# Kernel optimization log

Measured on AMD Instinct MI355X. Metric: run time of the kernel, lower is better.

Reference implementation:

```python
import jax, jax.numpy as jnp
import numpy as np

N_NODES = 50000
BN_EPS = 1e-5


def gcn_conv(x, W, b, src, dst):
    # PyG GCNConv: linear, add self-loops, symmetric degree normalization, scatter-add, bias.
    h = x @ W                                        # [N, D]
    n = x.shape[0]
    deg = jax.ops.segment_sum(jnp.ones(src.shape[0], x.dtype), dst,
                              num_segments=n) + 1.0  # +1 for self-loop
    dinv = jnp.where(deg > 0, jax.lax.rsqrt(deg), 0.0)
    norm = dinv[src] * dinv[dst]                     # [E]
    agg = jax.ops.segment_sum(h[src] * norm[:, None], dst, num_segments=n)
    agg = agg + h * (dinv * dinv)[:, None]           # self-loop contribution
    return agg + b


def batch_norm(x, gamma, beta):
    # training-mode BN over the node axis (biased variance, as torch)
    mu = jnp.mean(x, axis=0)
    var = jnp.mean((x - mu) ** 2, axis=0)
    return (x - mu) * jax.lax.rsqrt(var + BN_EPS) * gamma + beta


def setup_inputs() -> dict:
    key = jax.random.key(0)
    ks = jax.random.split(key, 8)
    D, C = 128, 10
    x = jax.random.normal(ks[0], (N_NODES, D), dtype=jnp.float32)
    edge_index = jax.random.randint(ks[1], (2, 640000), 0, N_NODES, dtype=jnp.int32)
    s = 1.0 / np.sqrt(D)
    return {
        "x": x,
        "edge_index": edge_index,
        "W1": jax.random.normal(ks[2], (D, D), dtype=jnp.float32) * s,
        "b1": jnp.zeros((D,), jnp.float32),
        "gamma1": jnp.ones((D,), jnp.float32),
        "beta1": jnp.zeros((D,), jnp.float32),
        "W2": jax.random.normal(ks[3], (D, D), dtype=jnp.float32) * s,
        "b2": jnp.zeros((D,), jnp.float32),
        "gamma2": jnp.ones((D,), jnp.float32),
        "beta2": jnp.zeros((D,), jnp.float32),
        "lin1_w": jax.random.normal(ks[4], (D, D), dtype=jnp.float32) * s,
        "lin1_b": jnp.zeros((D,), jnp.float32),
        "lin2_w": jax.random.normal(ks[5], (D, C), dtype=jnp.float32) * s,
        "lin2_b": jnp.zeros((C,), jnp.float32),
    }


def reference(x, edge_index, W1, b1, gamma1, beta1, W2, b2, gamma2, beta2,
              lin1_w, lin1_b, lin2_w, lin2_b):
    src, dst = edge_index[0], edge_index[1]
    # layer 1: GCNConv -> ReLU -> BN (dropout = identity at eval)
    h = jax.nn.relu(gcn_conv(x, W1, b1, src, dst))
    h = batch_norm(h, gamma1, beta1)
    # layer 2
    h = jax.nn.relu(gcn_conv(h, W2, b2, src, dst))
    h = batch_norm(h, gamma2, beta2)
    # MLP head
    h = jax.nn.relu(h @ lin1_w + lin1_b)
    logits = h @ lin2_w + lin2_b
    return jax.nn.log_softmax(logits, axis=-1)
```

## Files before the change

### kernel.cpp

```cpp
#include <hip/hip_runtime.h>
#include <hip/hip_bf16.h>
#include <math.h>

typedef unsigned int uint;
typedef unsigned short ushort;
using f32x4 = __attribute__((ext_vector_type(4))) float;
using s16x8 = __attribute__((ext_vector_type(8))) short;

#define NSLOT 64

__device__ __forceinline__ float bflo(uint u) { return __uint_as_float(u << 16); }
__device__ __forceinline__ float bfhi(uint u) { return __uint_as_float(u & 0xffff0000u); }
__device__ __forceinline__ ushort f2bf(float f) {
    uint u = __float_as_uint(f);
    return (ushort)((u + 0x7fffu + ((u >> 16) & 1u)) >> 16);
}
__device__ __forceinline__ float sel4f(float a, float b, float c, float d, int i) {
    float r = a; r = (i == 1) ? b : r; r = (i == 2) ? c : r; r = (i == 3) ? d : r; return r;
}
__device__ __forceinline__ int sel4i(int a, int b, int c, int d, int i) {
    int r = a; r = (i == 1) ? b : r; r = (i == 2) ? c : r; r = (i == 3) ? d : r; return r;
}


__global__ void deg_count(const int* __restrict__ dst, int* __restrict__ deg, int E) {
    int e = blockIdx.x * 256 + threadIdx.x;
    if (e < E) atomicAdd(&deg[dst[e]], 1);
}

__global__ __launch_bounds__(256) void deg_block_sum(const int* __restrict__ deg,
                                                     int* __restrict__ bsum, int N) {
    __shared__ int s[256];
    int i = blockIdx.x * 256 + threadIdx.x;
    s[threadIdx.x] = (i < N) ? deg[i] : 0;
    __syncthreads();
    #pragma unroll
    for (int off = 128; off > 0; off >>= 1) {
        if (threadIdx.x < off) s[threadIdx.x] += s[threadIdx.x + off];
        __syncthreads();
    }
    if (threadIdx.x == 0) bsum[blockIdx.x] = s[0];
}

__global__ __launch_bounds__(256) void scan_bsum(int* __restrict__ bsum, int nblk) {
    __shared__ int s[256];
    int t = threadIdx.x;
    s[t] = (t < nblk) ? bsum[t] : 0;
    __syncthreads();
    for (int off = 1; off < 256; off <<= 1) {
        int v = (t >= off) ? s[t - off] : 0;
        __syncthreads();
        s[t] += v;
        __syncthreads();
    }
    if (t < nblk) bsum[t] = (t == 0) ? 0 : s[t - 1];
}

__global__ __launch_bounds__(256) void fill_rowstart(const int* __restrict__ deg,
                                                     const int* __restrict__ bsum,
                                                     int* __restrict__ row_start,
                                                     int* __restrict__ cursor,
                                                     float* __restrict__ dinv, int N, int E) {
    __shared__ int s[256];
    int t = threadIdx.x;
    int i = blockIdx.x * 256 + t;
    int dg = (i < N) ? deg[i] : 0;
    s[t] = dg;
    __syncthreads();
    for (int off = 1; off < 256; off <<= 1) {
        int v = (t >= off) ? s[t - off] : 0;
        __syncthreads();
        s[t] += v;
        __syncthreads();
    }
    if (i < N) {
        int excl = bsum[blockIdx.x] + s[t] - dg;
        row_start[i] = excl;
        cursor[i] = excl;
        dinv[i] = rsqrtf((float)dg + 1.0f);
    }
    if (i == 0) row_start[N] = E;
}

__global__ void csr_fill(const int* __restrict__ src, const int* __restrict__ dst,
                         const float* __restrict__ dinv, int* __restrict__ cursor,
                         int2* __restrict__ csr2, int E) {
    int e = blockIdx.x * 256 + threadIdx.x;
    if (e >= E) return;
    int s = src[e], d = dst[e];
    int pos = atomicAdd(&cursor[d], 1);
    csr2[pos] = make_int2(s, __float_as_int(dinv[s] * dinv[d]));
}


__global__ __launch_bounds__(256) void prep_weights(const float* __restrict__ W1,
                                                    const float* __restrict__ W2,
                                                    const float* __restrict__ W3,
                                                    const float* __restrict__ l2w,
                                                    ushort* __restrict__ wt1,
                                                    ushort* __restrict__ wt2,
                                                    ushort* __restrict__ wt3,
                                                    float* __restrict__ w2t) {
    int i = blockIdx.x * 256 + threadIdx.x;
    int li = i & 16383;
    int k = li >> 7, n = li & 127;
    const float* Ws = (i < 16384) ? W1 : (i < 32768) ? W2 : W3;
    ushort* Wd = (i < 16384) ? wt1 : (i < 32768) ? wt2 : wt3;
    Wd[n * 128 + k] = f2bf(Ws[li]);
    if (i < 1280) {
        int kk = i / 10, c = i % 10;
        w2t[c * 128 + kk] = l2w[i];
    }
}


template<bool XF32, bool AFF, bool BIAS, bool RELU>
__global__ __launch_bounds__(256) void gemm_mfma(const void* __restrict__ Xv,
                                                 const float* __restrict__ scale,
                                                 const float* __restrict__ shift,
                                                 const ushort* __restrict__ Bt,
                                                 const float* __restrict__ bias,
                                                 ushort* __restrict__ Y, int N) {
    __shared__ char smem[16384 + 32768];
    char* Al = smem;
    char* Bl = smem + 16384;

    int tid = threadIdx.x;
    int brow = blockIdx.x * 64;

    {
        int n = tid >> 1, h = tid & 1;
        const uint4* srcp = (const uint4*)(Bt + n * 128 + h * 64);
        #pragma unroll
        for (int i = 0; i < 8; ++i) {
            uint4 v = srcp[i];
            int u = (h * 8 + i) ^ (n & 7);
            *(uint4*)(Bl + n * 256 + u * 16) = v;
        }
    }
    {
        int r = tid >> 2, c0 = (tid & 3) * 32;
        int row = brow + r;
        bool ok = row < N;
        uint pk[16];
        if (XF32) {
            const float* Xr = (const float*)Xv + (size_t)row * 128 + c0;
            #pragma unroll
            for (int i = 0; i < 16; ++i) {
                float f0 = ok ? Xr[i * 2] : 0.f;
                float f1 = ok ? Xr[i * 2 + 1] : 0.f;
                pk[i] = (uint)f2bf(f0) | ((uint)f2bf(f1) << 16);
            }
        } else {
            const uint* Xr = (const uint*)((const ushort*)Xv + (size_t)row * 128 + c0);
            #pragma unroll
            for (int i = 0; i < 16; ++i) {
                uint u = ok ? Xr[i] : 0u;
                float f0 = bflo(u), f1 = bfhi(u);
                if (AFF) {
                    int c = c0 + i * 2;
                    f0 = f0 * scale[c] + shift[c];
                    f1 = f1 * scale[c + 1] + shift[c + 1];
                }
                pk[i] = (uint)f2bf(f0) | ((uint)f2bf(f1) << 16);
            }
        }
        #pragma unroll
        for (int i = 0; i < 4; ++i) {
            int u = ((tid & 3) * 4 + i) ^ (r & 7);
            *(uint4*)(Al + r * 256 + u * 16) = *(uint4*)&pk[i * 4];
        }
    }
    __syncthreads();

    int lane = tid & 63, w = tid >> 6;
    int m = lane & 15, g = lane >> 4;
    int wr = w * 16;

    f32x4 acc[8];
    #pragma unroll
    for (int nt = 0; nt < 8; ++nt) acc[nt] = (f32x4){0.f, 0.f, 0.f, 0.f};

    #pragma unroll
    for (int kk = 0; kk < 4; ++kk) {
        int u = (kk * 4 + g) ^ (m & 7);
        s16x8 a = *(const s16x8*)(Al + (wr + m) * 256 + u * 16);
        #pragma unroll
        for (int nt = 0; nt < 8; ++nt) {
            s16x8 b = *(const s16x8*)(Bl + (nt * 16 + m) * 256 + u * 16);
            acc[nt] = __builtin_amdgcn_mfma_f32_16x16x32_bf16(a, b, acc[nt], 0, 0, 0);
        }
    }

    float bv[8];
    if (BIAS) {
        #pragma unroll
        for (int nt = 0; nt < 8; ++nt) bv[nt] = bias[nt * 16 + m];
    }
    #pragma unroll
    for (int i = 0; i < 4; ++i) {
        int row = brow + wr + g * 4 + i;
        if (row < N) {
            #pragma unroll
            for (int nt = 0; nt < 8; ++nt) {
                float v = acc[nt][i];
                if (BIAS) v += bv[nt];
                if (RELU) v = fmaxf(v, 0.f);
                Y[(size_t)row * 128 + nt * 16 + m] = f2bf(v);
            }
        }
    }
}


__global__ __launch_bounds__(256) void gather_fused(const ushort* __restrict__ H,
                                                    const int* __restrict__ row_start,
                                                    const int2* __restrict__ csr2,
                                                    const float* __restrict__ dinv,
                                                    const float* __restrict__ bias,
                                                    ushort* __restrict__ Y,
                                                    float* __restrict__ bnpart, int N) {
    int g = threadIdx.x >> 6, lane = threadIdx.x & 63;
    int d = lane * 2;
    float b0 = bias[d], b1 = bias[d + 1];
    float s0 = 0.f, s1 = 0.f, ss0 = 0.f, ss1 = 0.f;

    int nchunks = (N + 3) / 4;
    int chunk = blockIdx.x * 4 + g;

    if (chunk < nchunks) {
        int c = chunk * 4;
        int nn = min(4, N - c);

        int rsv = row_start[c + min(lane, nn)];
        int rs0 = __shfl(rsv, 0);
        int rs1 = __shfl(rsv, min(1, nn));
        int rs2 = __shfl(rsv, min(2, nn));
        int rs3 = __shfl(rsv, min(3, nn));
        int rs4 = __shfl(rsv, nn);

        float dvv = dinv[c + min(lane, nn - 1)];
        float dv0 = __shfl(dvv, 0);
        float dv1 = __shfl(dvv, min(1, nn - 1));
        float dv2 = __shfl(dvv, min(2, nn - 1));
        float dv3 = __shfl(dvv, min(3, nn - 1));

        uint h0 = *(const uint*)&H[(size_t)c * 128 + d];
        uint h1 = (nn > 1) ? *(const uint*)&H[(size_t)(c + 1) * 128 + d] : 0u;
        uint h2 = (nn > 2) ? *(const uint*)&H[(size_t)(c + 2) * 128 + d] : 0u;
        uint h3 = (nn > 3) ? *(const uint*)&H[(size_t)(c + 3) * 128 + d] : 0u;

        float i0_0 = bflo(h0) * dv0 * dv0 + b0, i1_0 = bfhi(h0) * dv0 * dv0 + b1;
        float i0_1 = bflo(h1) * dv1 * dv1 + b0, i1_1 = bfhi(h1) * dv1 * dv1 + b1;
        float i0_2 = bflo(h2) * dv2 * dv2 + b0, i1_2 = bfhi(h2) * dv2 * dv2 + b1;
        float i0_3 = bflo(h3) * dv3 * dv3 + b0, i1_3 = bfhi(h3) * dv3 * dv3 + b1;

        int e0 = rs0, eend = rs4;
        int seg = 0;
        int nextb = rs1;
        float a0 = i0_0, a1 = i1_0;

        for (int base = e0; base < eend; base += 64) {
            int cnt = min(64, eend - base);
            int2 me = (lane < cnt) ? csr2[base + lane] : make_int2(0, 0);
            int sl = me.x;
            float nl = __int_as_float(me.y);

            for (int j = 0; j < cnt; j += 8) {
                int mm = min(8, cnt - j);
                uint v[8]; float nr[8];
                #pragma unroll
                for (int k = 0; k < 8; ++k) {
                    int idx = min(j + k, cnt - 1);
                    int sk = __shfl(sl, idx);
                    float nk = __shfl(nl, idx);
                    nr[k] = (k < mm) ? nk : 0.f;
                    v[k] = *(const uint*)&H[(size_t)sk * 128 + d];
                }
                #pragma unroll
                for (int k = 0; k < 8; ++k) {
                    if (k < mm) {
                        int e = base + j + k;
                        while (e >= nextb) {
                            float r0 = fmaxf(a0, 0.f), r1 = fmaxf(a1, 0.f);
                            *(uint*)&Y[(size_t)(c + seg) * 128 + d] =
                                (uint)f2bf(r0) | ((uint)f2bf(r1) << 16);
                            s0 += r0; ss0 += r0 * r0; s1 += r1; ss1 += r1 * r1;
                            seg++;
                            a0 = sel4f(i0_0, i0_1, i0_2, i0_3, seg);
                            a1 = sel4f(i1_0, i1_1, i1_2, i1_3, seg);
                            nextb = sel4i(rs1, rs2, rs3, rs4, seg);
                        }
                        a0 += bflo(v[k]) * nr[k];
                        a1 += bfhi(v[k]) * nr[k];
                    }
                }
            }
        }
        for (;;) {
            float r0 = fmaxf(a0, 0.f), r1 = fmaxf(a1, 0.f);
            *(uint*)&Y[(size_t)(c + seg) * 128 + d] = (uint)f2bf(r0) | ((uint)f2bf(r1) << 16);
            s0 += r0; ss0 += r0 * r0; s1 += r1; ss1 += r1 * r1;
            seg++;
            if (seg >= nn) break;
            a0 = sel4f(i0_0, i0_1, i0_2, i0_3, seg);
            a1 = sel4f(i1_0, i1_1, i1_2, i1_3, seg);
            nextb = sel4i(rs1, rs2, rs3, rs4, seg);
        }
    }

    float* bp = bnpart + (size_t)(blockIdx.x & (NSLOT - 1)) * 256;
    __shared__ float red[4][128];
    red[g][d] = s0; red[g][d + 1] = s1;
    __syncthreads();
    if (g == 0) {
        atomicAdd(&bp[d],     red[0][d] + red[1][d] + red[2][d] + red[3][d]);
        atomicAdd(&bp[d + 1], red[0][d + 1] + red[1][d + 1] + red[2][d + 1] + red[3][d + 1]);
    }
    __syncthreads();
    red[g][d] = ss0; red[g][d + 1] = ss1;
    __syncthreads();
    if (g == 0) {
        atomicAdd(&bp[128 + d],     red[0][d] + red[1][d] + red[2][d] + red[3][d]);
        atomicAdd(&bp[128 + d + 1], red[0][d + 1] + red[1][d + 1] + red[2][d + 1] + red[3][d + 1]);
    }
}

__global__ void bnfinalize(float* __restrict__ bnpart,
                           const float* __restrict__ gamma, const float* __restrict__ beta,
                           float* __restrict__ scale, float* __restrict__ shift, float invN) {
    int d = threadIdx.x;
    float sum = 0.f, ss = 0.f;
    #pragma unroll 8
    for (int s = 0; s < NSLOT; ++s) {
        sum += bnpart[s * 256 + d];
        ss  += bnpart[s * 256 + 128 + d];
        bnpart[s * 256 + d] = 0.f;
        bnpart[s * 256 + 128 + d] = 0.f;
    }
    float mu  = sum * invN;
    float var = ss * invN - mu * mu;
    float sc  = gamma[d] * rsqrtf(var + 1e-5f);
    scale[d] = sc;
    shift[d] = beta[d] - mu * sc;
}


__global__ __launch_bounds__(256) void head_ls(const ushort* __restrict__ H,
                                               const float* __restrict__ W2t,
                                               const float* __restrict__ b2,
                                               float* __restrict__ OUT, int N) {
    int wv = threadIdx.x >> 6, lane = threadIdx.x & 63;
    int row = blockIdx.x * 4 + wv;
    if (row >= N) return;
    uint hv = *(const uint*)&H[(size_t)row * 128 + lane * 2];
    float h0 = bflo(hv), h1 = bfhi(hv);
    float logit[10];
    #pragma unroll
    for (int c = 0; c < 10; ++c) {
        float2 w = *(const float2*)&W2t[c * 128 + lane * 2];
        float p = h0 * w.x + h1 * w.y;
        #pragma unroll
        for (int off = 32; off > 0; off >>= 1) p += __shfl_xor(p, off, 64);
        logit[c] = p + b2[c];
    }
    float m = logit[0];
    #pragma unroll
    for (int c = 1; c < 10; ++c) m = fmaxf(m, logit[c]);
    float sum = 0.f;
    #pragma unroll
    for (int c = 0; c < 10; ++c) sum += expf(logit[c] - m);
    float lse = m + logf(sum);
    if (lane < 10) OUT[(size_t)row * 10 + lane] = logit[lane] - lse;
}


static inline char* align16(char* p) { return (char*)(((uintptr_t)p + 15) & ~(uintptr_t)15); }

extern "C" void kernel_launch(void* const* d_in, const int* in_sizes, int n_in,
                              void* d_out, int out_size, void* d_ws, size_t ws_size,
                              hipStream_t stream) {
    const float* x    = (const float*)d_in[0];
    const int*   ei   = (const int*)d_in[1];
    const float* W1   = (const float*)d_in[2];
    const float* b1   = (const float*)d_in[3];
    const float* g1   = (const float*)d_in[4];
    const float* be1  = (const float*)d_in[5];
    const float* W2   = (const float*)d_in[6];
    const float* b2   = (const float*)d_in[7];
    const float* g2   = (const float*)d_in[8];
    const float* be2  = (const float*)d_in[9];
    const float* l1w  = (const float*)d_in[10];
    const float* l1b  = (const float*)d_in[11];
    const float* l2w  = (const float*)d_in[12];
    const float* l2b  = (const float*)d_in[13];
    float* out = (float*)d_out;

    int N = in_sizes[0] / 128;
    int E = in_sizes[1] / 2;
    const int* srcp = ei;
    const int* dstp = ei + E;

    char* w = (char*)d_ws;
    ushort* bufA  = (ushort*)w;  w = align16(w + (size_t)N * 128 * 2);
    ushort* bufB  = (ushort*)w;  w = align16(w + (size_t)N * 128 * 2);
    int*   degc   = (int*)w;     w += (size_t)N * 4;
    float* bnpart = (float*)w;   w = align16(w + (size_t)NSLOT * 256 * 4);
    float* dinv   = (float*)w;   w = align16(w + (size_t)N * 4);
    int*   row_st = (int*)w;     w = align16(w + (size_t)(N + 1) * 4);
    int*   cursor = (int*)w;     w = align16(w + (size_t)N * 4);
    int*   bsum   = (int*)w;     w = align16(w + 256 * 4);
    int2*  csr2   = (int2*)w;    w = align16(w + (size_t)E * 8);
    float* scale  = (float*)w;   w = align16(w + 128 * 4);
    float* shift  = (float*)w;   w = align16(w + 128 * 4);
    float* w2t    = (float*)w;   w = align16(w + 1280 * 4);
    ushort* wt1   = (ushort*)w;  w = align16(w + 16384 * 2);
    ushort* wt2   = (ushort*)w;  w = align16(w + 16384 * 2);
    ushort* wt3   = (ushort*)w;  w = align16(w + 16384 * 2);

    int eg = (E + 255) / 256;
    int ng = (N + 255) / 256;
    int gemm_grid = (N + 63) / 64;
    int nchunks = (N + 3) / 4;
    int gather_grid = (nchunks + 3) / 4;

    hipMemsetAsync(degc, 0, ((size_t)N + NSLOT * 256) * 4, stream);
    deg_count<<<eg, 256, 0, stream>>>(dstp, degc, E);
    deg_block_sum<<<ng, 256, 0, stream>>>(degc, bsum, N);
    scan_bsum<<<1, 256, 0, stream>>>(bsum, ng);
    fill_rowstart<<<ng, 256, 0, stream>>>(degc, bsum, row_st, cursor, dinv, N, E);
    csr_fill<<<eg, 256, 0, stream>>>(srcp, dstp, dinv, cursor, csr2, E);
    prep_weights<<<192, 256, 0, stream>>>(W1, W2, l1w, l2w, wt1, wt2, wt3, w2t);

    gemm_mfma<true, false, false, false><<<gemm_grid, 256, 0, stream>>>(x, nullptr, nullptr, wt1, nullptr, bufA, N);
    gather_fused<<<gather_grid, 256, 0, stream>>>(bufA, row_st, csr2, dinv, b1, bufB, bnpart, N);
    bnfinalize<<<1, 128, 0, stream>>>(bnpart, g1, be1, scale, shift, 1.0f / N);

    gemm_mfma<false, true, false, false><<<gemm_grid, 256, 0, stream>>>(bufB, scale, shift, wt2, nullptr, bufA, N);
    gather_fused<<<gather_grid, 256, 0, stream>>>(bufA, row_st, csr2, dinv, b2, bufB, bnpart, N);
    bnfinalize<<<1, 128, 0, stream>>>(bnpart, g2, be2, scale, shift, 1.0f / N);

    gemm_mfma<false, true, true, true><<<gemm_grid, 256, 0, stream>>>(bufB, scale, shift, wt3, l1b, bufA, N);
    head_ls<<<(N + 3) / 4, 256, 0, stream>>>(bufA, w2t, l2b, out, N);
}
```

Measured before the change: 360.2 us.

## Fuse MLP head into last GEMM, merge block scan, widen gather batch

Three separate changes. The final log-softmax head now runs inside the last GEMM epilogue: the ReLU output is staged in shared memory as fp32 and each wave computes logits for its 16 rows, which removes one launch and a bf16 round trip through global memory. The single-block scan of block sums is folded into fill_rowstart, where every block rescans all block sums redundantly, removing one tiny launch. The gather loop now batches 16 neighbour loads instead of 8 to keep more memory requests in flight, at the cost of higher register pressure.

```diff
diff --git a/kernel.cpp b/kernel.cpp
--- a/kernel.cpp
+++ b/kernel.cpp
@@ -42,39 +42,31 @@
     if (threadIdx.x == 0) bsum[blockIdx.x] = s[0];
 }
 
-__global__ __launch_bounds__(256) void scan_bsum(int* __restrict__ bsum, int nblk) {
-    __shared__ int s[256];
-    int t = threadIdx.x;
-    s[t] = (t < nblk) ? bsum[t] : 0;
-    __syncthreads();
-    for (int off = 1; off < 256; off <<= 1) {
-        int v = (t >= off) ? s[t - off] : 0;
-        __syncthreads();
-        s[t] += v;
-        __syncthreads();
-    }
-    if (t < nblk) bsum[t] = (t == 0) ? 0 : s[t - 1];
-}
-
 __global__ __launch_bounds__(256) void fill_rowstart(const int* __restrict__ deg,
                                                      const int* __restrict__ bsum,
                                                      int* __restrict__ row_start,
                                                      int* __restrict__ cursor,
-                                                     float* __restrict__ dinv, int N, int E) {
+                                                     float* __restrict__ dinv,
+                                                     int N, int E, int nblk) {
     __shared__ int s[256];
+    __shared__ int sb[256];
     int t = threadIdx.x;
     int i = blockIdx.x * 256 + t;
     int dg = (i < N) ? deg[i] : 0;
     s[t] = dg;
+    sb[t] = (t < nblk) ? bsum[t] : 0;
     __syncthreads();
     for (int off = 1; off < 256; off <<= 1) {
-        int v = (t >= off) ? s[t - off] : 0;
+        int v1 = (t >= off) ? s[t - off] : 0;
+        int v2 = (t >= off) ? sb[t - off] : 0;
         __syncthreads();
-        s[t] += v;
+        s[t] += v1;
+        sb[t] += v2;
         __syncthreads();
     }
     if (i < N) {
-        int excl = bsum[blockIdx.x] + s[t] - dg;
+        int boff = (blockIdx.x == 0) ? 0 : sb[blockIdx.x - 1];
+        int excl = boff + s[t] - dg;
         row_start[i] = excl;
         cursor[i] = excl;
         dinv[i] = rsqrtf((float)dg + 1.0f);
@@ -114,13 +106,16 @@
 }
 
 
-template<bool XF32, bool AFF, bool BIAS, bool RELU>
+template<bool XF32, bool AFF, bool BIAS, bool RELU, bool HEAD>
 __global__ __launch_bounds__(256) void gemm_mfma(const void* __restrict__ Xv,
                                                  const float* __restrict__ scale,
                                                  const float* __restrict__ shift,
                                                  const ushort* __restrict__ Bt,
                                                  const float* __restrict__ bias,
-                                                 ushort* __restrict__ Y, int N) {
+                                                 ushort* __restrict__ Y,
+                                                 const float* __restrict__ W2t,
+                                                 const float* __restrict__ b2,
+                                                 float* __restrict__ OUT, int N) {
     __shared__ char smem[16384 + 32768];
     char* Al = smem;
     char* Bl = smem + 16384;
@@ -197,17 +192,56 @@
         #pragma unroll
         for (int nt = 0; nt < 8; ++nt) bv[nt] = bias[nt * 16 + m];
     }
-    #pragma unroll
-    for (int i = 0; i < 4; ++i) {
-        int row = brow + wr + g * 4 + i;
-        if (row < N) {
+
+    if (!HEAD) {
+        #pragma unroll
+        for (int i = 0; i < 4; ++i) {
+            int row = brow + wr + g * 4 + i;
+            if (row < N) {
+                #pragma unroll
+                for (int nt = 0; nt < 8; ++nt) {
+                    float v = acc[nt][i];
+                    if (BIAS) v += bv[nt];
+                    if (RELU) v = fmaxf(v, 0.f);
+                    Y[(size_t)row * 128 + nt * 16 + m] = f2bf(v);
+                }
+            }
+        }
+    } else {
+        float* hl = (float*)smem;
+        __syncthreads();
+        #pragma unroll
+        for (int i = 0; i < 4; ++i) {
+            int r = wr + g * 4 + i;
             #pragma unroll
             for (int nt = 0; nt < 8; ++nt) {
                 float v = acc[nt][i];
                 if (BIAS) v += bv[nt];
                 if (RELU) v = fmaxf(v, 0.f);
-                Y[(size_t)row * 128 + nt * 16 + m] = f2bf(v);
-            }
+                hl[r * 132 + nt * 16 + m] = v;
+            }
+        }
+        __syncthreads();
+        for (int r = 0; r < 16; ++r) {
+            int grow = brow + wr + r;
+            float2 h2 = *(const float2*)&hl[(wr + r) * 132 + lane * 2];
+            float logit[10];
+            #pragma unroll
+            for (int c = 0; c < 10; ++c) {
+                float2 wv = *(const float2*)&W2t[c * 128 + lane * 2];
+                float p = h2.x * wv.x + h2.y * wv.y;
+                #pragma unroll
+                for (int off = 32; off > 0; off >>= 1) p += __shfl_xor(p, off, 64);
+                logit[c] = p + b2[c];
+            }
+            float mx = logit[0];
+            #pragma unroll
+            for (int c = 1; c < 10; ++c) mx = fmaxf(mx, logit[c]);
+            float sum = 0.f;
+            #pragma unroll
+            for (int c = 0; c < 10; ++c) sum += expf(logit[c] - mx);
+            float lse = mx + logf(sum);
+            if (lane < 10 && grow < N) OUT[(size_t)grow * 10 + lane] = logit[lane] - lse;
         }
     }
 }
@@ -266,11 +300,11 @@
             int sl = me.x;
             float nl = __int_as_float(me.y);
 
-            for (int j = 0; j < cnt; j += 8) {
-                int mm = min(8, cnt - j);
-                uint v[8]; float nr[8];
+            for (int j = 0; j < cnt; j += 16) {
+                int mm = min(16, cnt - j);
+                uint v[16]; float nr[16];
                 #pragma unroll
-                for (int k = 0; k < 8; ++k) {
+                for (int k = 0; k < 16; ++k) {
                     int idx = min(j + k, cnt - 1);
                     int sk = __shfl(sl, idx);
                     float nk = __shfl(nl, idx);
@@ -278,7 +312,7 @@
                     v[k] = *(const uint*)&H[(size_t)sk * 128 + d];
                 }
                 #pragma unroll
-                for (int k = 0; k < 8; ++k) {
+                for (int k = 0; k < 16; ++k) {
                     if (k < mm) {
                         int e = base + j + k;
                         while (e >= nextb) {
@@ -343,35 +377,6 @@
     float sc  = gamma[d] * rsqrtf(var + 1e-5f);
     scale[d] = sc;
     shift[d] = beta[d] - mu * sc;
-}
-
-
-__global__ __launch_bounds__(256) void head_ls(const ushort* __restrict__ H,
-                                               const float* __restrict__ W2t,
-                                               const float* __restrict__ b2,
-                                               float* __restrict__ OUT, int N) {
-    int wv = threadIdx.x >> 6, lane = threadIdx.x & 63;
-    int row = blockIdx.x * 4 + wv;
-    if (row >= N) return;
-    uint hv = *(const uint*)&H[(size_t)row * 128 + lane * 2];
-    float h0 = bflo(hv), h1 = bfhi(hv);
-    float logit[10];
-    #pragma unroll
-    for (int c = 0; c < 10; ++c) {
-        float2 w = *(const float2*)&W2t[c * 128 + lane * 2];
-        float p = h0 * w.x + h1 * w.y;
-        #pragma unroll
-        for (int off = 32; off > 0; off >>= 1) p += __shfl_xor(p, off, 64);
-        logit[c] = p + b2[c];
-    }
-    float m = logit[0];
-    #pragma unroll
-    for (int c = 1; c < 10; ++c) m = fmaxf(m, logit[c]);
-    float sum = 0.f;
-    #pragma unroll
-    for (int c = 0; c < 10; ++c) sum += expf(logit[c] - m);
-    float lse = m + logf(sum);
-    if (lane < 10) OUT[(size_t)row * 10 + lane] = logit[lane] - lse;
 }
 
 
@@ -427,19 +432,20 @@
     hipMemsetAsync(degc, 0, ((size_t)N + NSLOT * 256) * 4, stream);
     deg_count<<<eg, 256, 0, stream>>>(dstp, degc, E);
     deg_block_sum<<<ng, 256, 0, stream>>>(degc, bsum, N);
-    scan_bsum<<<1, 256, 0, stream>>>(bsum, ng);
-    fill_rowstart<<<ng, 256, 0, stream>>>(degc, bsum, row_st, cursor, dinv, N, E);
+    fill_rowstart<<<ng, 256, 0, stream>>>(degc, bsum, row_st, cursor, dinv, N, E, ng);
     csr_fill<<<eg, 256, 0, stream>>>(srcp, dstp, dinv, cursor, csr2, E);
     prep_weights<<<192, 256, 0, stream>>>(W1, W2, l1w, l2w, wt1, wt2, wt3, w2t);
 
-    gemm_mfma<true, false, false, false><<<gemm_grid, 256, 0, stream>>>(x, nullptr, nullptr, wt1, nullptr, bufA, N);
+    gemm_mfma<true, false, false, false, false><<<gemm_grid, 256, 0, stream>>>(
+        x, nullptr, nullptr, wt1, nullptr, bufA, nullptr, nullptr, nullptr, N);
     gather_fused<<<gather_grid, 256, 0, stream>>>(bufA, row_st, csr2, dinv, b1, bufB, bnpart, N);
     bnfinalize<<<1, 128, 0, stream>>>(bnpart, g1, be1, scale, shift, 1.0f / N);
 
-    gemm_mfma<false, true, false, false><<<gemm_grid, 256, 0, stream>>>(bufB, scale, shift, wt2, nullptr, bufA, N);
+    gemm_mfma<false, true, false, false, false><<<gemm_grid, 256, 0, stream>>>(
+        bufB, scale, shift, wt2, nullptr, bufA, nullptr, nullptr, nullptr, N);
     gather_fused<<<gather_grid, 256, 0, stream>>>(bufA, row_st, csr2, dinv, b2, bufB, bnpart, N);
     bnfinalize<<<1, 128, 0, stream>>>(bnpart, g2, be2, scale, shift, 1.0f / N);
 
-    gemm_mfma<false, true, true, true><<<gemm_grid, 256, 0, stream>>>(bufB, scale, shift, wt3, l1b, bufA, N);
-    head_ls<<<(N + 3) / 4, 256, 0, stream>>>(bufA, w2t, l2b, out, N);
-}
+    gemm_mfma<false, true, true, true, true><<<gemm_grid, 256, 0, stream>>>(
+        bufB, scale, shift, wt3, l1b, nullptr, w2t, l2b, out, N);
+}
```

Result: no change. 364.2 us (+1.1%).
